# Performance work log

Hardware: AMD Instinct MI355X
Metric: run time of the kernel (lower is better)

Reference implementation:

```python
import math
import jax, jax.numpy as jnp
import numpy as np

N_WIRES = 12
N_LAYERS = 3
BATCH = 2048
DIM = 2 ** N_WIRES


def _apply_1q(psi, U, wire):
    # psi: (B, 2^n) complex; U: (2,2) or (B,2,2)
    B = psi.shape[0]
    left = 2 ** wire
    psi = psi.reshape(B, left, 2, -1)
    if U.ndim == 3:
        psi = jnp.einsum('bij,bajc->baic', U, psi)
    else:
        psi = jnp.einsum('ij,bajc->baic', U, psi)
    return psi.reshape(B, -1)


def _apply_cnot(psi, wire):
    # CNOT on (control=wire, target=wire+1), adjacent wires
    B = psi.shape[0]
    left = 2 ** wire
    psi = psi.reshape(B, left, 2, 2, -1)
    flipped = psi[:, :, 1, ::-1, :][:, :, None]   # control=1 branch, target flipped
    psi = jnp.concatenate([psi[:, :, 0:1], flipped], axis=2)
    return psi.reshape(B, -1)


def _ry(theta):
    # RY(t) = [[cos t/2, -sin t/2],[sin t/2, cos t/2]]; theta: () or (B,)
    c = jnp.cos(theta / 2)
    s = jnp.sin(theta / 2)
    U = jnp.stack([jnp.stack([c, -s], -1), jnp.stack([s, c], -1)], -2)
    return U.astype(jnp.complex64)


def _rz(theta):
    # RZ(t) = diag(e^{-it/2}, e^{it/2}); theta scalar
    em = jnp.exp(-0.5j * theta.astype(jnp.complex64))
    ep = jnp.exp(0.5j * theta.astype(jnp.complex64))
    e00 = jnp.array([[1, 0], [0, 0]], dtype=jnp.complex64)
    e11 = jnp.array([[0, 0], [0, 1]], dtype=jnp.complex64)
    return e00 * em + e11 * ep


def _measure_z(psi):
    # <Z_w> for every wire; psi: (B, 2^n)
    B = psi.shape[0]
    p = jnp.abs(psi) ** 2
    outs = []
    for w in range(N_WIRES):
        pr = p.reshape(B, 2 ** w, 2, -1)
        outs.append(pr[:, :, 0].sum((1, 2)) - pr[:, :, 1].sum((1, 2)))
    return jnp.stack(outs, axis=-1)  # (B, n_wires)


def _forward(x, W1, b1, ry_theta, rz_theta, W2, b2):
    feat = x @ W1.T + b1                      # (B, n_wires)
    angles = jnp.tanh(feat) * math.pi         # encoding angles
    B = x.shape[0]
    psi = jnp.zeros((B, DIM), dtype=jnp.complex64).at[:, 0].set(1.0)
    # data encoding: per-sample RY on each wire
    for w in range(N_WIRES):
        psi = _apply_1q(psi, _ry(angles[:, w]), w)
    # variational layers with SHARED ry/rz params (module reuse in torch code)
    Ury = _ry(ry_theta)
    Urz = _rz(rz_theta)
    for _ in range(N_LAYERS):
        for w in range(N_WIRES):
            psi = _apply_1q(psi, Ury, w)
            psi = _apply_1q(psi, Urz, w)
        for w in range(N_WIRES - 1):
            psi = _apply_cnot(psi, w)
    z = _measure_z(psi)                        # (B, n_wires) real
    return z @ W2.T + b2                       # (B, 10) logits


def setup_inputs() -> dict:
    key = jax.random.key(0)
    ks = jax.random.split(key, 7)
    return {
        'x': jax.random.normal(ks[0], (BATCH, 784), dtype=jnp.float32),
        'W1': jax.random.normal(ks[1], (N_WIRES, 784), dtype=jnp.float32) * 0.03,
        'b1': jnp.zeros((N_WIRES,), dtype=jnp.float32),
        'ry_theta': jax.random.uniform(ks[2], (), dtype=jnp.float32) * 2 * math.pi,
        'rz_theta': jax.random.uniform(ks[3], (), dtype=jnp.float32) * 2 * math.pi,
        'W2': jax.random.normal(ks[4], (10, N_WIRES), dtype=jnp.float32) * 0.2,
        'b2': jnp.zeros((10,), dtype=jnp.float32),
    }


def reference(x, W1, b1, ry_theta, rz_theta, W2, b2):
    return _forward(x, W1, b1, ry_theta, rz_theta, W2, b2)
```

## Files before the change

### kernel.cpp

```cpp
#include <hip/hip_runtime.h>
#include <math.h>

#define NW   12
#define DIM  4096
#define TPB  256

typedef float v2f __attribute__((ext_vector_type(2)));

template<int CTRL>
__device__ __forceinline__ float fdpp(float v) {
    union { float f; int i; } u, w;
    u.f = v;
    w.i = __builtin_amdgcn_update_dpp(0, u.i, CTRL, 0xF, 0xF, false);
    return w.f;
}

template<int B>
__device__ __forceinline__ void ry_reg(v2f* r, float c, v2f vps, v2f vms) {
#pragma unroll
    for (int p = 0; p < 8; ++p) {
        const int i0 = ((p >> B) << (B + 1)) | (p & ((1 << B) - 1));
        const int i1 = i0 | (1 << B);
        const v2f a = r[i0], b = r[i1];
        r[i0] = __builtin_elementwise_fma(vms, b, a * c);
        r[i1] = __builtin_elementwise_fma(vps, a, b * c);
    }
}

template<int CTRL>
__device__ __forceinline__ void ry_dpp(v2f* r, float c, v2f vsp) {
#pragma unroll
    for (int k = 0; k < 16; ++k) {
        const v2f p = { fdpp<CTRL>(r[k].x), fdpp<CTRL>(r[k].y) };
        r[k] = __builtin_elementwise_fma(vsp, p, r[k] * c);
    }
}

__global__ __launch_bounds__(TPB, 4)
void qmnist_kernel(const float* __restrict__ x,  const float* __restrict__ W1,
                   const float* __restrict__ b1, const float* __restrict__ ryp,
                   const float* __restrict__ rzp, const float* __restrict__ W2,
                   const float* __restrict__ b2, float* __restrict__ out) {
    __shared__ v2f psi[DIM];
    float* smf  = (float*)psi;
    float* wred = smf;
    float* encc = smf + 48;
    float* encs = smf + 60;
    float* zfin = smf + 72;

    const int tid  = threadIdx.x;
    const int blk  = blockIdx.x;
    const int lane = tid & 63;
    const int wave = tid >> 6;

    float acc[NW];
#pragma unroll
    for (int w = 0; w < NW; ++w) acc[w] = 0.f;
    if (tid < 196) {
        const float4 xv = ((const float4*)(x + (size_t)blk * 784))[tid];
#pragma unroll
        for (int w = 0; w < NW; ++w) {
            const float4 wv = ((const float4*)(W1 + w * 784))[tid];
            acc[w] = fmaf(xv.x, wv.x, fmaf(xv.y, wv.y, fmaf(xv.z, wv.z, xv.w * wv.w)));
        }
    }
#pragma unroll
    for (int w = 0; w < NW; ++w) {
        float v = acc[w];
        v += __shfl_down(v, 32);
        v += __shfl_down(v, 16);
        v += __shfl_down(v, 8);
        v += __shfl_down(v, 4);
        v += __shfl_down(v, 2);
        v += __shfl_down(v, 1);
        if (lane == 0) wred[wave * NW + w] = v;
    }
    __syncthreads();
    if (tid < NW) {
        float feat = wred[tid] + wred[NW + tid] + wred[2 * NW + tid] + wred[3 * NW + tid] + b1[tid];
        float a = tanhf(feat) * 3.14159265358979323846f;
        float h = 0.5f * a;
        encc[tid] = cosf(h);
        encs[tid] = sinf(h);
    }
    __syncthreads();

    float hi = 1.f;
#pragma unroll
    for (int b = 0; b < 8; ++b)
        hi *= ((tid >> b) & 1) ? encs[11 - b] : encc[11 - b];
    v2f r[16];
#pragma unroll
    for (int k = 0; k < 16; ++k) {
        float f = hi;
        f *= (k & 1) ? encs[3] : encc[3];
        f *= (k & 2) ? encs[2] : encc[2];
        f *= (k & 4) ? encs[1] : encc[1];
        f *= (k & 8) ? encs[0] : encc[0];
        r[k] = (v2f){ f, 0.f };
    }

    const float ry = ryp[0], rz = rzp[0];
    const float c = cosf(0.5f * ry), s = sinf(0.5f * ry);
    const v2f vps = {  s,  s };
    const v2f vms = { -s, -s };
    const int pcT = __popc(tid);
    v2f qv[5], qp[5];
#pragma unroll
    for (int j = 0; j < 5; ++j) {
        const float ang = rz * (float)(pcT + j - 6);
        const float qc = cosf(ang), qs = sinf(ang);
        qv[j] = (v2f){  qc, qs };
        qp[j] = (v2f){ -qs, qc };
    }

    const v2f vs0 = (lane & 1)  ? vps : vms;
    const v2f vs1 = (lane & 2)  ? vps : vms;
    const v2f vs3 = (lane & 8)  ? vps : vms;
    const v2f vs5 = (lane & 32) ? vps : vms;

    const int t0 = tid & 1,        t1 = (tid >> 1) & 1, t2 = (tid >> 2) & 1,
              t3 = (tid >> 3) & 1, t4 = (tid >> 4) & 1, t5 = (tid >> 5) & 1;
    const int wbaseA = (tid & 3) | (t3 << 2) | (t5 << 3) | (t2 << 4) | (t4 << 5) | (tid & 192);
    const int rbaseA = (tid & 3) | (t3 << 2) | (t5 << 3) | (t2 << 8) | (t4 << 9) | ((tid & 192) << 4);
    const int wbaseC = (tid & 3) | (t3 << 2) | (t5 << 3) | (t2 << 4) | (t4 << 5) | ((tid & 192) << 4);
    const int gt = tid ^ (tid >> 1);
    const int rbaseC0 = (gt & 1) | (((gt >> 1) & 1) << 1) | (((gt >> 3) & 1) << 2) |
                        (((gt >> 5) & 1) << 3) | (((gt >> 2) & 1) << 6) |
                        (((gt >> 4) & 1) << 7) | (((gt >> 6) & 1) << 8) | (((gt >> 7) & 1) << 9);
    const int rbaseC1 = rbaseC0 ^ 512;

    for (int layer = 0; layer < 3; ++layer) {
        __syncthreads();

        ry_reg<0>(r, c, vps, vms); ry_reg<1>(r, c, vps, vms);
        ry_reg<2>(r, c, vps, vms); ry_reg<3>(r, c, vps, vms);

        ry_dpp<0xB1>(r, c, vs0);
        ry_dpp<0x4E>(r, c, vs1);
        ry_dpp<0x128>(r, c, vs3);
#pragma unroll
        for (int k = 0; k < 16; ++k) {
            const v2f p = { __shfl_xor(r[k].x, 32, 64), __shfl_xor(r[k].y, 32, 64) };
            r[k] = __builtin_elementwise_fma(vs5, p, r[k] * c);
        }

#pragma unroll
        for (int k = 0; k < 16; ++k)
            psi[wbaseA + (k << 8)] = r[k];
        __syncthreads();
#pragma unroll
        for (int k = 0; k < 16; ++k)
            r[k] = psi[rbaseA + (k << 4)];

        ry_reg<0>(r, c, vps, vms); ry_reg<1>(r, c, vps, vms);
        ry_reg<2>(r, c, vps, vms); ry_reg<3>(r, c, vps, vms);

#pragma unroll
        for (int k = 0; k < 16; ++k) {
            const int j = __popc(k);
            r[k] = __builtin_elementwise_fma((v2f){ r[k].y, r[k].y }, qp[j], qv[j] * r[k].x);
        }

        __syncthreads();
#pragma unroll
        for (int k = 0; k < 16; ++k)
            psi[wbaseC + (k << 6)] = r[k];
        __syncthreads();
#pragma unroll
        for (int k = 0; k < 16; ++k) {
            const int gk   = (k ^ (k >> 1)) & 15;
            const int immC = ((gk & 3) << 4) | ((gk & 12) << 8);
            r[k] = psi[((k & 1) ? rbaseC1 : rbaseC0) + immC];
        }
    }
    __syncthreads();

    float t_total = 0.f, s3 = 0.f, s2 = 0.f, s1 = 0.f, s0 = 0.f;
#pragma unroll
    for (int k = 0; k < 16; ++k) {
        const float pp = fmaf(r[k].x, r[k].x, r[k].y * r[k].y);
        t_total += pp;
        if (k & 1) s3 += pp;
        if (k & 2) s2 += pp;
        if (k & 4) s1 += pp;
        if (k & 8) s0 += pp;
    }
    float contrib[NW];
    contrib[3] = t_total - 2.f * s3;
    contrib[2] = t_total - 2.f * s2;
    contrib[1] = t_total - 2.f * s1;
    contrib[0] = t_total - 2.f * s0;
#pragma unroll
    for (int b = 0; b < 8; ++b) {
        const int w = 11 - b;
        contrib[w] = ((tid >> b) & 1) ? -t_total : t_total;
    }
#pragma unroll
    for (int w = 0; w < NW; ++w) {
        float v = contrib[w];
        v += __shfl_down(v, 32);
        v += __shfl_down(v, 16);
        v += __shfl_down(v, 8);
        v += __shfl_down(v, 4);
        v += __shfl_down(v, 2);
        v += __shfl_down(v, 1);
        if (lane == 0) wred[wave * NW + w] = v;
    }
    __syncthreads();
    if (tid < NW)
        zfin[tid] = wred[tid] + wred[NW + tid] + wred[2 * NW + tid] + wred[3 * NW + tid];
    __syncthreads();

    if (tid < 10) {
        float o = b2[tid];
#pragma unroll
        for (int w = 0; w < NW; ++w)
            o = fmaf(zfin[w], W2[tid * NW + w], o);
        out[(size_t)blk * 10 + tid] = o;
    }
}

extern "C" void kernel_launch(void* const* d_in, const int* in_sizes, int n_in,
                              void* d_out, int out_size, void* d_ws, size_t ws_size,
                              hipStream_t stream) {
    const float* x   = (const float*)d_in[0];
    const float* W1  = (const float*)d_in[1];
    const float* b1  = (const float*)d_in[2];
    const float* ry  = (const float*)d_in[3];
    const float* rz  = (const float*)d_in[4];
    const float* W2  = (const float*)d_in[5];
    const float* b2  = (const float*)d_in[6];
    float* out = (float*)d_out;

    const int batch = in_sizes[0] / 784;
    qmnist_kernel<<<batch, TPB, 0, stream>>>(x, W1, b1, ry, rz, W2, b2, out);
}
```

Before: 123.3 us.

## Do more RY wires in registers via cross-lane permutes, drop one LDS transpose

Wires whose amplitudes live across lanes 4 and 16 now go through DPP and permlane16/32 swaps instead of an LDS round trip. This lets each layer use a simpler two-phase shared-memory exchange with a direct tid-indexed layout, removing one barrier and the old swizzled addressing. Fewer register-resident RY passes run after the first transpose. The new plain layouts may bring LDS bank conflicts, and the permlane builtins fall back to swizzle or shuffle if they are unavailable.

```diff
diff --git a/kernel.cpp b/kernel.cpp
--- a/kernel.cpp
+++ b/kernel.cpp
@@ -6,6 +6,7 @@
 #define TPB  256
 
 typedef float v2f __attribute__((ext_vector_type(2)));
+typedef unsigned v2u __attribute__((ext_vector_type(2)));
 
 template<int CTRL>
 __device__ __forceinline__ float fdpp(float v) {
@@ -15,6 +16,26 @@
     return w.f;
 }
 
+__device__ __forceinline__ float xor16f(float v, bool hi) {
+#if __has_builtin(__builtin_amdgcn_permlane16_swap)
+    const v2u pr = __builtin_amdgcn_permlane16_swap(__float_as_uint(v), __float_as_uint(v), false, false);
+    return __uint_as_float(hi ? pr.x : pr.y);
+#else
+    union { float f; int i; } u, w;
+    u.f = v;
+    w.i = __builtin_amdgcn_ds_swizzle(u.i, 0x401F);
+    return w.f;
+#endif
+}
+__device__ __forceinline__ float xor32f(float v, bool hi) {
+#if __has_builtin(__builtin_amdgcn_permlane32_swap)
+    const v2u pr = __builtin_amdgcn_permlane32_swap(__float_as_uint(v), __float_as_uint(v), false, false);
+    return __uint_as_float(hi ? pr.x : pr.y);
+#else
+    return __shfl_xor(v, 32, 64);
+#endif
+}
+
 template<int B>
 __device__ __forceinline__ void ry_reg(v2f* r, float c, v2f vps, v2f vms) {
 #pragma unroll
@@ -32,6 +53,15 @@
 #pragma unroll
     for (int k = 0; k < 16; ++k) {
         const v2f p = { fdpp<CTRL>(r[k].x), fdpp<CTRL>(r[k].y) };
+        r[k] = __builtin_elementwise_fma(vsp, p, r[k] * c);
+    }
+}
+
+__device__ __forceinline__ void ry_xor4(v2f* r, float c, v2f vsp) {
+#pragma unroll
+    for (int k = 0; k < 16; ++k) {
+        const v2f p = { fdpp<0x141>(fdpp<0x1B>(r[k].x)),
+                        fdpp<0x141>(fdpp<0x1B>(r[k].y)) };
         r[k] = __builtin_elementwise_fma(vsp, p, r[k] * c);
     }
 }
@@ -116,45 +146,44 @@
 
     const v2f vs0 = (lane & 1)  ? vps : vms;
     const v2f vs1 = (lane & 2)  ? vps : vms;
+    const v2f vs2 = (lane & 4)  ? vps : vms;
     const v2f vs3 = (lane & 8)  ? vps : vms;
+    const v2f vs4 = (lane & 16) ? vps : vms;
     const v2f vs5 = (lane & 32) ? vps : vms;
-
-    const int t0 = tid & 1,        t1 = (tid >> 1) & 1, t2 = (tid >> 2) & 1,
-              t3 = (tid >> 3) & 1, t4 = (tid >> 4) & 1, t5 = (tid >> 5) & 1;
-    const int wbaseA = (tid & 3) | (t3 << 2) | (t5 << 3) | (t2 << 4) | (t4 << 5) | (tid & 192);
-    const int rbaseA = (tid & 3) | (t3 << 2) | (t5 << 3) | (t2 << 8) | (t4 << 9) | ((tid & 192) << 4);
-    const int wbaseC = (tid & 3) | (t3 << 2) | (t5 << 3) | (t2 << 4) | (t4 << 5) | ((tid & 192) << 4);
-    const int gt = tid ^ (tid >> 1);
-    const int rbaseC0 = (gt & 1) | (((gt >> 1) & 1) << 1) | (((gt >> 3) & 1) << 2) |
-                        (((gt >> 5) & 1) << 3) | (((gt >> 2) & 1) << 6) |
-                        (((gt >> 4) & 1) << 7) | (((gt >> 6) & 1) << 8) | (((gt >> 7) & 1) << 9);
-    const int rbaseC1 = rbaseC0 ^ 512;
+    const bool h4 = (lane & 16) != 0;
+    const bool h5 = (lane & 32) != 0;
+
+    const int rb1 = (tid & 63) | ((tid & 192) << 2);
+    const int gt  = tid ^ (tid >> 1);
 
     for (int layer = 0; layer < 3; ++layer) {
-        __syncthreads();
-
         ry_reg<0>(r, c, vps, vms); ry_reg<1>(r, c, vps, vms);
         ry_reg<2>(r, c, vps, vms); ry_reg<3>(r, c, vps, vms);
-
         ry_dpp<0xB1>(r, c, vs0);
         ry_dpp<0x4E>(r, c, vs1);
+        ry_xor4(r, c, vs2);
         ry_dpp<0x128>(r, c, vs3);
 #pragma unroll
         for (int k = 0; k < 16; ++k) {
-            const v2f p = { __shfl_xor(r[k].x, 32, 64), __shfl_xor(r[k].y, 32, 64) };
+            const v2f p = { xor16f(r[k].x, h4), xor16f(r[k].y, h4) };
+            r[k] = __builtin_elementwise_fma(vs4, p, r[k] * c);
+        }
+#pragma unroll
+        for (int k = 0; k < 16; ++k) {
+            const v2f p = { xor32f(r[k].x, h5), xor32f(r[k].y, h5) };
             r[k] = __builtin_elementwise_fma(vs5, p, r[k] * c);
         }
 
+        __syncthreads();
 #pragma unroll
         for (int k = 0; k < 16; ++k)
-            psi[wbaseA + (k << 8)] = r[k];
+            psi[(k << 8) | tid] = r[k];
         __syncthreads();
 #pragma unroll
         for (int k = 0; k < 16; ++k)
-            r[k] = psi[rbaseA + (k << 4)];
+            r[k] = psi[rb1 | ((k & 3) << 6) | ((k >> 2) << 10)];
 
         ry_reg<0>(r, c, vps, vms); ry_reg<1>(r, c, vps, vms);
-        ry_reg<2>(r, c, vps, vms); ry_reg<3>(r, c, vps, vms);
 
 #pragma unroll
         for (int k = 0; k < 16; ++k) {
@@ -162,16 +191,14 @@
             r[k] = __builtin_elementwise_fma((v2f){ r[k].y, r[k].y }, qp[j], qv[j] * r[k].x);
         }
 
+#pragma unroll
+        for (int k = 0; k < 16; ++k)
+            psi[rb1 | ((k & 3) << 6) | ((k >> 2) << 10)] = r[k];
         __syncthreads();
 #pragma unroll
-        for (int k = 0; k < 16; ++k)
-            psi[wbaseC + (k << 6)] = r[k];
-        __syncthreads();
-#pragma unroll
-        for (int k = 0; k < 16; ++k) {
-            const int gk   = (k ^ (k >> 1)) & 15;
-            const int immC = ((gk & 3) << 4) | ((gk & 12) << 8);
-            r[k] = psi[((k & 1) ? rbaseC1 : rbaseC0) + immC];
+        for (int k = 0; k < 16; ++k) {
+            const int gk = (k ^ (k >> 1)) & 15;
+            r[k] = psi[(gt ^ ((k & 1) << 7)) | (gk << 8)];
         }
     }
     __syncthreads();
```

Result: no change. 125.6 us (+1.9%).

## Restructure LDS exchange layout and use DPP for stride-4 lane butterfly

Applied to the files above, without the earlier changes.

Reworks how the statevector is partitioned between registers, lanes and LDS across the gate stages. The lanes now hold wires 0-3 (lane bits) and registers hold the others, which replaces the cross-half shfl_xor 32 with a two-step DPP xor-4 permute. The permuted LDS index formulas become simpler tid-based addressing, and one barrier is dropped because the post-RZ write reuses the same addresses that thread just read. The new linear layouts may introduce LDS bank conflicts compared with the earlier swizzled bases.

```diff
diff --git a/kernel.cpp b/kernel.cpp
--- a/kernel.cpp
+++ b/kernel.cpp
@@ -32,6 +32,15 @@
 #pragma unroll
     for (int k = 0; k < 16; ++k) {
         const v2f p = { fdpp<CTRL>(r[k].x), fdpp<CTRL>(r[k].y) };
+        r[k] = __builtin_elementwise_fma(vsp, p, r[k] * c);
+    }
+}
+
+__device__ __forceinline__ void ry_xor4(v2f* r, float c, v2f vsp) {
+#pragma unroll
+    for (int k = 0; k < 16; ++k) {
+        const v2f p = { fdpp<0x141>(fdpp<0x1B>(r[k].x)),
+                        fdpp<0x141>(fdpp<0x1B>(r[k].y)) };
         r[k] = __builtin_elementwise_fma(vsp, p, r[k] * c);
     }
 }
@@ -114,44 +123,30 @@
         qp[j] = (v2f){ -qs, qc };
     }
 
-    const v2f vs0 = (lane & 1)  ? vps : vms;
-    const v2f vs1 = (lane & 2)  ? vps : vms;
-    const v2f vs3 = (lane & 8)  ? vps : vms;
-    const v2f vs5 = (lane & 32) ? vps : vms;
-
-    const int t0 = tid & 1,        t1 = (tid >> 1) & 1, t2 = (tid >> 2) & 1,
-              t3 = (tid >> 3) & 1, t4 = (tid >> 4) & 1, t5 = (tid >> 5) & 1;
-    const int wbaseA = (tid & 3) | (t3 << 2) | (t5 << 3) | (t2 << 4) | (t4 << 5) | (tid & 192);
-    const int rbaseA = (tid & 3) | (t3 << 2) | (t5 << 3) | (t2 << 8) | (t4 << 9) | ((tid & 192) << 4);
-    const int wbaseC = (tid & 3) | (t3 << 2) | (t5 << 3) | (t2 << 4) | (t4 << 5) | ((tid & 192) << 4);
-    const int gt = tid ^ (tid >> 1);
-    const int rbaseC0 = (gt & 1) | (((gt >> 1) & 1) << 1) | (((gt >> 3) & 1) << 2) |
-                        (((gt >> 5) & 1) << 3) | (((gt >> 2) & 1) << 6) |
-                        (((gt >> 4) & 1) << 7) | (((gt >> 6) & 1) << 8) | (((gt >> 7) & 1) << 9);
-    const int rbaseC1 = rbaseC0 ^ 512;
+    const v2f vs0 = (lane & 1) ? vps : vms;
+    const v2f vs1 = (lane & 2) ? vps : vms;
+    const v2f vs2 = (lane & 4) ? vps : vms;
+    const v2f vs3 = (lane & 8) ? vps : vms;
+
+    const int base_r = (tid & 15) | ((tid & 240) << 4);
+    const int gt     = tid ^ (tid >> 1);
 
     for (int layer = 0; layer < 3; ++layer) {
-        __syncthreads();
-
         ry_reg<0>(r, c, vps, vms); ry_reg<1>(r, c, vps, vms);
         ry_reg<2>(r, c, vps, vms); ry_reg<3>(r, c, vps, vms);
-
         ry_dpp<0xB1>(r, c, vs0);
         ry_dpp<0x4E>(r, c, vs1);
+        ry_xor4(r, c, vs2);
         ry_dpp<0x128>(r, c, vs3);
-#pragma unroll
-        for (int k = 0; k < 16; ++k) {
-            const v2f p = { __shfl_xor(r[k].x, 32, 64), __shfl_xor(r[k].y, 32, 64) };
-            r[k] = __builtin_elementwise_fma(vs5, p, r[k] * c);
-        }
-
+
+        __syncthreads();
 #pragma unroll
         for (int k = 0; k < 16; ++k)
-            psi[wbaseA + (k << 8)] = r[k];
+            psi[(k << 8) | tid] = r[k];
         __syncthreads();
 #pragma unroll
         for (int k = 0; k < 16; ++k)
-            r[k] = psi[rbaseA + (k << 4)];
+            r[k] = psi[base_r | (k << 4)];
 
         ry_reg<0>(r, c, vps, vms); ry_reg<1>(r, c, vps, vms);
         ry_reg<2>(r, c, vps, vms); ry_reg<3>(r, c, vps, vms);
@@ -162,16 +157,14 @@
             r[k] = __builtin_elementwise_fma((v2f){ r[k].y, r[k].y }, qp[j], qv[j] * r[k].x);
         }
 
+#pragma unroll
+        for (int k = 0; k < 16; ++k)
+            psi[base_r | (k << 4)] = r[k];
         __syncthreads();
 #pragma unroll
-        for (int k = 0; k < 16; ++k)
-            psi[wbaseC + (k << 6)] = r[k];
-        __syncthreads();
-#pragma unroll
         for (int k = 0; k < 16; ++k) {
-            const int gk   = (k ^ (k >> 1)) & 15;
-            const int immC = ((gk & 3) << 4) | ((gk & 12) << 8);
-            r[k] = psi[((k & 1) ? rbaseC1 : rbaseC0) + immC];
+            const int gk = (k ^ (k >> 1)) & 15;
+            r[k] = psi[(gt ^ ((k & 1) << 7)) | (gk << 8)];
         }
     }
     __syncthreads();
```

New measurement: 115.9 us. 6.1% less time.
